# Optimization experiments

Measured on AMD Instinct MI355X. Metric: run time of the kernel, lower is better.

The kernel has to match this reference:

```python
import jax, jax.numpy as jnp
from jax import lax
import numpy as np

B = 8192   # samples
L = 32     # predicted chars per sample (num_chars[i])
M = 32     # target labels per sample (num_labels[i])
C = 96     # character classes


def _edit_trace(pred, tgt):
    """Levenshtein DP + backtrace for one sample.
    pred: [L] int, tgt: [M] int.
    Returns (ti, tj, valid) of length L+M: 1-based (i,j) positions of the
    diagonal (match/substitute) moves on the optimal edit path, as emitted by
    distance_and_trace; valid masks non-diagonal / out-of-path steps."""
    Ls, Ms = pred.shape[0], tgt.shape[0]
    cost = (pred[:, None] != tgt[None, :]).astype(jnp.int32)  # [L,M]
    row0 = jnp.arange(Ms + 1, dtype=jnp.int32)

    def row_step(prev, crow):
        first = prev[0] + 1
        def col_step(left, z):
            up, diag, c = z
            v = jnp.minimum(jnp.minimum(up + 1, left + 1), diag + c)
            return v, v
        _, rest = lax.scan(col_step, first, (prev[1:], prev[:-1], crow))
        new = jnp.concatenate([first[None], rest])
        return new, new

    _, rows = lax.scan(row_step, row0, cost)
    D = jnp.concatenate([row0[None, :], rows], axis=0)  # [L+1, M+1]

    def bt_step(carry, _):
        i, j = carry
        c = cost[jnp.maximum(i - 1, 0), jnp.maximum(j - 1, 0)]
        dij = D[i, j]
        diag = (i > 0) & (j > 0) & (D[i - 1, j - 1] + c == dij)
        up = (~diag) & (i > 0) & (D[i - 1, j] + 1 == dij)
        left = (~diag) & (~up) & (j > 0)
        ni = i - (diag | up).astype(jnp.int32)
        nj = j - (diag | left).astype(jnp.int32)
        return (ni, nj), (i, j, diag)

    (_, _), (ti, tj, valid) = lax.scan(
        bt_step, (jnp.int32(Ls), jnp.int32(Ms)), None, length=Ls + Ms)
    return ti, tj, valid


def _forward(x, y, num_chars, num_labels):
    b = num_chars.shape[0]
    c = x.shape[1]
    l = x.shape[0] // b
    m = y.shape[0] // b
    logits = x.reshape(b, l, c)          # [B,L,C]
    labels = y.reshape(b, m)             # [B,M]
    pred = jnp.argmax(logits, axis=-1)   # torch.max(x,1) indices
    ti, tj, valid = jax.vmap(_edit_trace)(pred, labels)  # [B, L+M] each
    logp = jax.nn.log_softmax(logits, axis=-1)
    xi = jnp.where(valid, ti - 1, 0)     # trace[:,0]-1 (+ per-sample offset via reshape)
    yi = jnp.where(valid, tj - 1, 0)     # trace[:,1]-1
    lab = jnp.take_along_axis(labels, yi, axis=1)                 # [B,L+M]
    lp = jnp.take_along_axis(logp, xi[..., None], axis=1)         # [B,L+M,C]
    ce = -jnp.take_along_axis(lp, lab[..., None], axis=2)[..., 0]  # [B,L+M]
    cnt = valid.sum(axis=1)
    per_sample = jnp.where(valid, ce, 0.0).sum(axis=1) / jnp.maximum(cnt, 1)
    nonempty = cnt > 0                   # attenuation: skip empty traces
    total = jnp.where(nonempty, per_sample, 0.0).sum()
    return total / nonempty.sum()


def setup_inputs() -> dict:
    key = jax.random.key(0)
    k1, k2 = jax.random.split(key)
    x = jax.random.normal(k1, (B * L, C), dtype=jnp.float32)
    y = jax.random.randint(k2, (B * M,), 0, C, dtype=jnp.int32)
    num_chars = jnp.full((B,), L, dtype=jnp.int32)
    num_labels = jnp.full((B,), M, dtype=jnp.int32)
    return {"x": x, "y": y, "num_chars": num_chars, "num_labels": num_labels}


def reference(x, y, num_chars, num_labels):
    return _forward(x, y, num_chars, num_labels)
```

## Files before the change

### kernel.cpp

```cpp
#include <hip/hip_runtime.h>
#include <stdint.h>

#define BNUM  8192
#define LROWS 32
#define MLAB  32
#define CCLS  96
#define WPB   4
#define SPW   2
#define SPB   (WPB*SPW)
#define NBLK  (BNUM/SPB)

__device__ __forceinline__ int dpp_wshr1_i32(int v) {
    return __builtin_amdgcn_update_dpp(0, v, 0x138, 0xF, 0xF, true);
}
__device__ __forceinline__ float dpp_wshr1_f32(float v) {
    return __int_as_float(
        __builtin_amdgcn_update_dpp(0, __float_as_int(v), 0x138, 0xF, 0xF, true));
}

__global__ __launch_bounds__(256, 4) void editloss_main(
    const float* __restrict__ x, const int* __restrict__ y,
    float* __restrict__ partial_sum, float* __restrict__ partial_cnt)
{
    __shared__ float  ceTab[SPB][LROWS * MLAB];
    __shared__ float2 lpS[SPB][LROWS];
    __shared__ float  psum[SPB];
    __shared__ float  pcnt[SPB];

    const int w    = threadIdx.x >> 6;
    const int lane = threadIdx.x & 63;
    const int g    = lane >> 5;
    const int u    = lane & 31;
    const int s    = w * SPW + g;
    const int sb   = blockIdx.x * SPB + s;

    const float* xs    = x + (size_t)sb * (LROWS * CCLS);
    const int    lab_u = y[sb * MLAB + u];

    {
        const float4* rowv = (const float4*)(xs + (size_t)u * CCLS);
        float bmax[4]; int bidx[4]; float bsum[4];
#pragma unroll
        for (int c = 0; c < 4; ++c) { bmax[c] = -1e30f; bidx[c] = 0; bsum[c] = 0.f; }

        float4 va[24];
#pragma unroll
        for (int t = 0; t < 24; ++t) va[t] = rowv[t];

#pragma unroll
        for (int t = 0; t < 24; ++t) {
            const int c = t / 6;
            const float4 v = va[t];
            const int base = t * 4;
            if (v.x > bmax[c]) { bmax[c] = v.x; bidx[c] = base + 0; }
            if (v.y > bmax[c]) { bmax[c] = v.y; bidx[c] = base + 1; }
            if (v.z > bmax[c]) { bmax[c] = v.z; bidx[c] = base + 2; }
            if (v.w > bmax[c]) { bmax[c] = v.w; bidx[c] = base + 3; }
            bsum[c] += __expf(v.x) + __expf(v.y) + __expf(v.z) + __expf(v.w);
        }
        float m = bmax[0]; int idx = bidx[0];
#pragma unroll
        for (int c = 1; c < 4; ++c)
            if (bmax[c] > m) { m = bmax[c]; idx = bidx[c]; }
        const float lse = __logf((bsum[0] + bsum[1]) + (bsum[2] + bsum[3]));
        lpS[s][u] = make_float2(lse, (float)idx);
    }
    asm volatile("s_waitcnt lgkmcnt(0)" ::: "memory");

    {
        const float* gcol = xs + lab_u;
#pragma unroll
        for (int r = 0; r < LROWS; ++r) {
            const float2 lp = lpS[s][r];
            const float  xg = gcol[r * CCLS];
            const float  ce = lp.x - xg;
            ceTab[s][r * MLAB + u] = ((int)lp.y == lab_u) ? ce : -ce;
        }
    }
    asm volatile("s_waitcnt lgkmcnt(0)" ::: "memory");

    const int j = u + 1;
    int   prevW = 0;   float prevCE = 0.f;
    int   diagW = 0;   float diagCE = 0.f;
#pragma unroll 4
    for (int d = 1; d <= LROWS + MLAB; ++d) {
        const int   lWs  = dpp_wshr1_i32(prevW);
        const float lCEs = dpp_wshr1_f32(prevCE);
        const int i = d - j;
        const int   lW  = (u == 0) ? max(i, 0)     : lWs;
        const float lCE = (u == 0) ? 0.f           : lCEs;
        const int   dW  = (u == 0) ? max(i - 1, 0) : diagW;
        const float dCE = (u == 0) ? 0.f           : diagCE;
        int curW; float curCE;
        if (i <= 0) {
            curW = j; curCE = 0.f;
        } else if (i > LROWS) {
            curW = prevW; curCE = prevCE;
        } else {
            const int uD = prevW & 255, uC = prevW >> 8;
            const int lD = lW & 255,    lC = lW >> 8;
            const int dD = dW & 255,    dC = dW >> 8;
            const float ct  = ceTab[s][(i - 1) * MLAB + u];
            const int   c   = (ct < 0.f) ? 1 : 0;
            const int nD = min(min(uD, lD) + 1, dD + c);
            const bool dg = (dD + c == nD);
            const bool up = !dg && (uD + 1 == nD);
            int nC; float nCE;
            if (dg)      { nC = dC + 1; nCE = dCE + fabsf(ct); }
            else if (up) { nC = uC;     nCE = prevCE;          }
            else         { nC = lC;     nCE = lCE;             }
            curW = nD | (nC << 8);
            curCE = nCE;
        }
        diagW = lWs; diagCE = lCEs;
        prevW = curW; prevCE = curCE;
    }

    if (u == 31) {
        const int cnt = prevW >> 8;
        psum[s] = (cnt > 0) ? prevCE / (float)cnt : 0.f;
        pcnt[s] = (cnt > 0) ? 1.f : 0.f;
    }
    __syncthreads();
    if (threadIdx.x == 0) {
        float ss = 0.f, cc = 0.f;
#pragma unroll
        for (int k = 0; k < SPB; ++k) { ss += psum[k]; cc += pcnt[k]; }
        partial_sum[blockIdx.x] = ss;
        partial_cnt[blockIdx.x] = cc;
    }
}

__global__ __launch_bounds__(256) void editloss_finalize(
    const float* __restrict__ partial_sum, const float* __restrict__ partial_cnt,
    float* __restrict__ out, int nblocks)
{
    float s = 0.f, c = 0.f;
    for (int k = threadIdx.x; k < nblocks; k += 256) {
        s += partial_sum[k];
        c += partial_cnt[k];
    }
#pragma unroll
    for (int d = 32; d >= 1; d >>= 1) {
        s += __shfl_xor(s, d);
        c += __shfl_xor(c, d);
    }
    __shared__ float ss[4], cc[4];
    const int w = threadIdx.x >> 6, lane = threadIdx.x & 63;
    if (lane == 0) { ss[w] = s; cc[w] = c; }
    __syncthreads();
    if (threadIdx.x == 0) {
        const float S  = ss[0] + ss[1] + ss[2] + ss[3];
        const float C2 = cc[0] + cc[1] + cc[2] + cc[3];
        out[0] = (C2 > 0.f) ? (S / C2) : 0.f;
    }
}

extern "C" void kernel_launch(void* const* d_in, const int* in_sizes, int n_in,
                              void* d_out, int out_size, void* d_ws, size_t ws_size,
                              hipStream_t stream) {
    const float* x = (const float*)d_in[0];
    const int*   y = (const int*)d_in[1];
    float* out = (float*)d_out;

    float* partial_sum = (float*)d_ws;
    float* partial_cnt = partial_sum + NBLK;

    editloss_main<<<NBLK, 256, 0, stream>>>(x, y, partial_sum, partial_cnt);
    editloss_finalize<<<1, 256, 0, stream>>>(partial_sum, partial_cnt, out, NBLK);
}
```

Measured before the change: 166.0 us.

## Stage logits through padded LDS with coalesced loads and fuse CE into DP

Switches to one-wavefront blocks of two samples. All logits are loaded with fully coalesced float4 reads into a padded shared-memory tile, replacing per-lane strided row loads and the strided label-column gather. The precomputed CE table is dropped, and CE plus the mismatch flag are computed inside the anti-diagonal DP from staged row data. The block reduction becomes a shuffle instead of a barrier. The cost is more LDS traffic inside the DP loop, scalar LDS writes during staging, and far more blocks.

```diff
diff --git a/kernel.cpp b/kernel.cpp
--- a/kernel.cpp
+++ b/kernel.cpp
@@ -5,10 +5,13 @@
 #define LROWS 32
 #define MLAB  32
 #define CCLS  96
-#define WPB   4
-#define SPW   2
-#define SPB   (WPB*SPW)
+#define SPB   2
 #define NBLK  (BNUM/SPB)
+#define PSTR  97
+#define SSTR  (LROWS*PSTR)
+#define XS_F  (SPB*SSTR)
+#define LP_F  XS_F
+#define TOT_F (XS_F + SPB*LROWS*2)
 
 __device__ __forceinline__ int dpp_wshr1_i32(int v) {
     return __builtin_amdgcn_update_dpp(0, v, 0x138, 0xF, 0xF, true);
@@ -18,75 +21,78 @@
         __builtin_amdgcn_update_dpp(0, __float_as_int(v), 0x138, 0xF, 0xF, true));
 }
 
-__global__ __launch_bounds__(256, 4) void editloss_main(
+__global__ __launch_bounds__(64, 2) void editloss_main(
     const float* __restrict__ x, const int* __restrict__ y,
     float* __restrict__ partial_sum, float* __restrict__ partial_cnt)
 {
-    __shared__ float  ceTab[SPB][LROWS * MLAB];
-    __shared__ float2 lpS[SPB][LROWS];
-    __shared__ float  psum[SPB];
-    __shared__ float  pcnt[SPB];
+    __shared__ float S[TOT_F];
 
-    const int w    = threadIdx.x >> 6;
-    const int lane = threadIdx.x & 63;
+    const int lane = threadIdx.x;
     const int g    = lane >> 5;
     const int u    = lane & 31;
-    const int s    = w * SPW + g;
-    const int sb   = blockIdx.x * SPB + s;
+    const int sb0  = blockIdx.x * SPB;
 
-    const float* xs    = x + (size_t)sb * (LROWS * CCLS);
-    const int    lab_u = y[sb * MLAB + u];
+    const float* gx    = x + (size_t)sb0 * (LROWS * CCLS);
+    const int    lab_u = y[(sb0 + g) * MLAB + u];
+
+#pragma unroll
+    for (int i = 0; i < 24; ++i) {
+        const int    f = i * 256 + lane * 4;
+        const float4 v = *(const float4*)(gx + f);
+        const int samp = (f >= 3072) ? 1 : 0;
+        const int fs   = f - samp * 3072;
+        const int n    = fs >> 5;
+        const int row  = (n * 171) >> 9;
+        const int col  = fs - row * 96;
+        float* p = &S[samp * SSTR + row * PSTR + col];
+        p[0] = v.x; p[1] = v.y; p[2] = v.z; p[3] = v.w;
+    }
+    asm volatile("s_waitcnt lgkmcnt(0)" ::: "memory");
 
     {
-        const float4* rowv = (const float4*)(xs + (size_t)u * CCLS);
+        const float* rp = &S[g * SSTR + u * PSTR];
         float bmax[4]; int bidx[4]; float bsum[4];
 #pragma unroll
         for (int c = 0; c < 4; ++c) { bmax[c] = -1e30f; bidx[c] = 0; bsum[c] = 0.f; }
-
-        float4 va[24];
-#pragma unroll
-        for (int t = 0; t < 24; ++t) va[t] = rowv[t];
-
 #pragma unroll
         for (int t = 0; t < 24; ++t) {
             const int c = t / 6;
-            const float4 v = va[t];
+            const float v0 = rp[t * 4 + 0];
+            const float v1 = rp[t * 4 + 1];
+            const float v2 = rp[t * 4 + 2];
+            const float v3 = rp[t * 4 + 3];
             const int base = t * 4;
-            if (v.x > bmax[c]) { bmax[c] = v.x; bidx[c] = base + 0; }
-            if (v.y > bmax[c]) { bmax[c] = v.y; bidx[c] = base + 1; }
-            if (v.z > bmax[c]) { bmax[c] = v.z; bidx[c] = base + 2; }
-            if (v.w > bmax[c]) { bmax[c] = v.w; bidx[c] = base + 3; }
-            bsum[c] += __expf(v.x) + __expf(v.y) + __expf(v.z) + __expf(v.w);
+            if (v0 > bmax[c]) { bmax[c] = v0; bidx[c] = base + 0; }
+            if (v1 > bmax[c]) { bmax[c] = v1; bidx[c] = base + 1; }
+            if (v2 > bmax[c]) { bmax[c] = v2; bidx[c] = base + 2; }
+            if (v3 > bmax[c]) { bmax[c] = v3; bidx[c] = base + 3; }
+            bsum[c] += __expf(v0) + __expf(v1) + __expf(v2) + __expf(v3);
         }
         float m = bmax[0]; int idx = bidx[0];
 #pragma unroll
         for (int c = 1; c < 4; ++c)
             if (bmax[c] > m) { m = bmax[c]; idx = bidx[c]; }
         const float lse = __logf((bsum[0] + bsum[1]) + (bsum[2] + bsum[3]));
-        lpS[s][u] = make_float2(lse, (float)idx);
+        S[LP_F + (g * 32 + u) * 2 + 0] = lse;
+        S[LP_F + (g * 32 + u) * 2 + 1] = (float)idx;
     }
     asm volatile("s_waitcnt lgkmcnt(0)" ::: "memory");
 
-    {
-        const float* gcol = xs + lab_u;
-#pragma unroll
-        for (int r = 0; r < LROWS; ++r) {
-            const float2 lp = lpS[s][r];
-            const float  xg = gcol[r * CCLS];
-            const float  ce = lp.x - xg;
-            ceTab[s][r * MLAB + u] = ((int)lp.y == lab_u) ? ce : -ce;
-        }
-    }
-    asm volatile("s_waitcnt lgkmcnt(0)" ::: "memory");
-
-    const int j = u + 1;
+    const int   j      = u + 1;
+    const float fl     = (float)lab_u;
+    const int   xbase  = g * SSTR + lab_u;
+    const int   lpbase = LP_F + g * 64;
     int   prevW = 0;   float prevCE = 0.f;
     int   diagW = 0;   float diagCE = 0.f;
 #pragma unroll 4
     for (int d = 1; d <= LROWS + MLAB; ++d) {
         const int   lWs  = dpp_wshr1_i32(prevW);
         const float lCEs = dpp_wshr1_f32(prevCE);
-        const int i = d - j;
+        const int i  = d - j;
+        const int ic = min(max(i - 1, 0), LROWS - 1);
+        const float xg  = S[xbase  + ic * PSTR];
+        const float lse = S[lpbase + ic * 2 + 0];
+        const float prf = S[lpbase + ic * 2 + 1];
         const int   lW  = (u == 0) ? max(i, 0)     : lWs;
         const float lCE = (u == 0) ? 0.f           : lCEs;
         const int   dW  = (u == 0) ? max(i - 1, 0) : diagW;
@@ -100,15 +106,15 @@
             const int uD = prevW & 255, uC = prevW >> 8;
             const int lD = lW & 255,    lC = lW >> 8;
             const int dD = dW & 255,    dC = dW >> 8;
-            const float ct  = ceTab[s][(i - 1) * MLAB + u];
-            const int   c   = (ct < 0.f) ? 1 : 0;
+            const float ce = lse - xg;
+            const int   c  = (prf != fl) ? 1 : 0;
             const int nD = min(min(uD, lD) + 1, dD + c);
             const bool dg = (dD + c == nD);
             const bool up = !dg && (uD + 1 == nD);
             int nC; float nCE;
-            if (dg)      { nC = dC + 1; nCE = dCE + fabsf(ct); }
-            else if (up) { nC = uC;     nCE = prevCE;          }
-            else         { nC = lC;     nCE = lCE;             }
+            if (dg)      { nC = dC + 1; nCE = dCE + ce; }
+            else if (up) { nC = uC;     nCE = prevCE;   }
+            else         { nC = lC;     nCE = lCE;      }
             curW = nD | (nC << 8);
             curCE = nCE;
         }
@@ -116,18 +122,17 @@
         prevW = curW; prevCE = curCE;
     }
 
+    float ps = 0.f, pc = 0.f;
     if (u == 31) {
         const int cnt = prevW >> 8;
-        psum[s] = (cnt > 0) ? prevCE / (float)cnt : 0.f;
-        pcnt[s] = (cnt > 0) ? 1.f : 0.f;
+        ps = (cnt > 0) ? prevCE / (float)cnt : 0.f;
+        pc = (cnt > 0) ? 1.f : 0.f;
     }
-    __syncthreads();
-    if (threadIdx.x == 0) {
-        float ss = 0.f, cc = 0.f;
-#pragma unroll
-        for (int k = 0; k < SPB; ++k) { ss += psum[k]; cc += pcnt[k]; }
-        partial_sum[blockIdx.x] = ss;
-        partial_cnt[blockIdx.x] = cc;
+    ps += __shfl_down(ps, 32);
+    pc += __shfl_down(pc, 32);
+    if (lane == 31) {
+        partial_sum[blockIdx.x] = ps;
+        partial_cnt[blockIdx.x] = pc;
     }
 }
 
@@ -166,6 +171,6 @@
     float* partial_sum = (float*)d_ws;
     float* partial_cnt = partial_sum + NBLK;
 
-    editloss_main<<<NBLK, 256, 0, stream>>>(x, y, partial_sum, partial_cnt);
+    editloss_main<<<NBLK, 64, 0, stream>>>(x, y, partial_sum, partial_cnt);
     editloss_finalize<<<1, 256, 0, stream>>>(partial_sum, partial_cnt, out, NBLK);
 }
```

After: 184.1 us. +10.8%, slower.

## Stage logits via async global-to-LDS loads with swizzle, split rows across half-waves

Applied to the files above, without the earlier changes.

Each wave now streams one sample's 32x96 logits straight into LDS with global_load_lds, using a swizzled layout to avoid bank conflicts. The row argmax and log-sum-exp is split across two half-waves and combined with a shuffle. After a barrier, half the waves exit and the rest run the DP for two samples per wave, reading labels' logits from LDS instead of global memory. Partial results are now written per sample, so the finalize kernel reduces over all 8192 samples. This aims to coalesce the global loads and drop the second strided gather, at the cost of idle waves during the DP, lower occupancy (launch bounds 3), and a larger final reduction.

```diff
diff --git a/kernel.cpp b/kernel.cpp
--- a/kernel.cpp
+++ b/kernel.cpp
@@ -5,10 +5,12 @@
 #define LROWS 32
 #define MLAB  32
 #define CCLS  96
-#define WPB   4
-#define SPW   2
-#define SPB   (WPB*SPW)
+#define SPB   4
 #define NBLK  (BNUM/SPB)
+#define XFL   (LROWS*CCLS)
+#define SFL   (XFL + 2*LROWS)
+
+typedef float f32x4 __attribute__((ext_vector_type(4)));
 
 __device__ __forceinline__ int dpp_wshr1_i32(int v) {
     return __builtin_amdgcn_update_dpp(0, v, 0x138, 0xF, 0xF, true);
@@ -18,68 +20,115 @@
         __builtin_amdgcn_update_dpp(0, __float_as_int(v), 0x138, 0xF, 0xF, true));
 }
 
-__global__ __launch_bounds__(256, 4) void editloss_main(
+__device__ __forceinline__ int swz12(int k, int r) {
+    return (k < 8) ? (k ^ (r & 7)) : (8 + ((k - 8) ^ (r & 3)));
+}
+
+__device__ __forceinline__ void gload16(const float* g, float* l) {
+    __builtin_amdgcn_global_load_lds(
+        (const __attribute__((address_space(1))) unsigned int*)g,
+        (__attribute__((address_space(3))) unsigned int*)l,
+        16, 0, 0);
+}
+
+__global__ __launch_bounds__(256, 3) void editloss_main(
     const float* __restrict__ x, const int* __restrict__ y,
     float* __restrict__ partial_sum, float* __restrict__ partial_cnt)
 {
-    __shared__ float  ceTab[SPB][LROWS * MLAB];
-    __shared__ float2 lpS[SPB][LROWS];
-    __shared__ float  psum[SPB];
-    __shared__ float  pcnt[SPB];
-
-    const int w    = threadIdx.x >> 6;
-    const int lane = threadIdx.x & 63;
-    const int g    = lane >> 5;
-    const int u    = lane & 31;
-    const int s    = w * SPW + g;
-    const int sb   = blockIdx.x * SPB + s;
-
-    const float* xs    = x + (size_t)sb * (LROWS * CCLS);
-    const int    lab_u = y[sb * MLAB + u];
+    __shared__ float S[SPB * SFL];
+
+    const int tid  = threadIdx.x;
+    const int w    = tid >> 6;
+    const int lane = tid & 63;
+    const int r    = lane & 31;
+    const int h    = lane >> 5;
+
+    const int    sb = blockIdx.x * SPB + w;
+    const float* gx = x + (size_t)sb * XFL;
+    float*       Sw = &S[w * SFL];
+
+#pragma unroll
+    for (int t = 0; t < 12; ++t) {
+        const int q   = t * 64 + lane;
+        const int rr  = (q * 683) >> 14;
+        const int rem = q - rr * 24;
+        const int hh  = (rem >= 12) ? 1 : 0;
+        const int kp  = rem - 12 * hh;
+        const int kk  = swz12(kp, rr);
+        const int G   = rr * 24 + 12 * hh + kk;
+        gload16(gx + G * 4, Sw + t * 256);
+    }
+    asm volatile("s_waitcnt vmcnt(0)" ::: "memory");
 
     {
-        const float4* rowv = (const float4*)(xs + (size_t)u * CCLS);
-        float bmax[4]; int bidx[4]; float bsum[4];
-#pragma unroll
-        for (int c = 0; c < 4; ++c) { bmax[c] = -1e30f; bidx[c] = 0; bsum[c] = 0.f; }
-
-        float4 va[24];
-#pragma unroll
-        for (int t = 0; t < 24; ++t) va[t] = rowv[t];
-
-#pragma unroll
-        for (int t = 0; t < 24; ++t) {
-            const int c = t / 6;
-            const float4 v = va[t];
-            const int base = t * 4;
-            if (v.x > bmax[c]) { bmax[c] = v.x; bidx[c] = base + 0; }
-            if (v.y > bmax[c]) { bmax[c] = v.y; bidx[c] = base + 1; }
-            if (v.z > bmax[c]) { bmax[c] = v.z; bidx[c] = base + 2; }
-            if (v.w > bmax[c]) { bmax[c] = v.w; bidx[c] = base + 3; }
-            bsum[c] += __expf(v.x) + __expf(v.y) + __expf(v.z) + __expf(v.w);
-        }
-        float m = bmax[0]; int idx = bidx[0];
-#pragma unroll
-        for (int c = 1; c < 4; ++c)
-            if (bmax[c] > m) { m = bmax[c]; idx = bidx[c]; }
-        const float lse = __logf((bsum[0] + bsum[1]) + (bsum[2] + bsum[3]));
-        lpS[s][u] = make_float2(lse, (float)idx);
+        f32x4 va[12];
+#pragma unroll
+        for (int k = 0; k < 12; ++k) {
+            const int p = r * 24 + h * 12 + swz12(k, r);
+            va[k] = *(const f32x4*)(Sw + p * 4);
+        }
+        float bmA = -1e30f, bmB = -1e30f; int biA = 0, biB = 0;
+        float bsA = 0.f, bsB = 0.f;
+#pragma unroll
+        for (int k = 0; k < 12; ++k) {
+            const f32x4 v = va[k];
+            const int base = h * 48 + k * 4;
+            if (k < 6) {
+                if (v[0] > bmA) { bmA = v[0]; biA = base + 0; }
+                if (v[1] > bmA) { bmA = v[1]; biA = base + 1; }
+                if (v[2] > bmA) { bmA = v[2]; biA = base + 2; }
+                if (v[3] > bmA) { bmA = v[3]; biA = base + 3; }
+                bsA += __expf(v[0]) + __expf(v[1]) + __expf(v[2]) + __expf(v[3]);
+            } else {
+                if (v[0] > bmB) { bmB = v[0]; biB = base + 0; }
+                if (v[1] > bmB) { bmB = v[1]; biB = base + 1; }
+                if (v[2] > bmB) { bmB = v[2]; biB = base + 2; }
+                if (v[3] > bmB) { bmB = v[3]; biB = base + 3; }
+                bsB += __expf(v[0]) + __expf(v[1]) + __expf(v[2]) + __expf(v[3]);
+            }
+        }
+        float mL = bmA; int iL = biA;
+        if (bmB > mL) { mL = bmB; iL = biB; }
+        const float sL = bsA + bsB;
+        const float mP = __shfl_xor(mL, 32);
+        const int   iP = __shfl_xor(iL, 32);
+        const float sP = __shfl_xor(sL, 32);
+        const float mLo = h ? mP : mL;  const int iLo = h ? iP : iL;
+        const float mHi = h ? mL : mP;  const int iHi = h ? iL : iP;
+        const float sLo = h ? sP : sL;  const float sHi = h ? sL : sP;
+        float m = mLo; int idx = iLo;
+        if (mHi > m) { m = mHi; idx = iHi; }
+        const float lse = __logf(sLo + sHi);
+        if (h == 0) {
+            Sw[XFL + r * 2 + 0] = lse;
+            Sw[XFL + r * 2 + 1] = (float)idx;
+        }
+    }
+    __syncthreads();
+    if (w >= 2) return;
+
+    const int    sLoc = w * 2 + h;
+    const int    samp = blockIdx.x * SPB + sLoc;
+    float*       Sg   = &S[sLoc * SFL];
+    const int    lab  = y[samp * MLAB + r];
+    {
+        const int   hh = (lab >= 48) ? 1 : 0;
+        const int   kq = (lab - 48 * hh) >> 2;
+        const int   el = lab & 3;
+        const float fl = (float)lab;
+#pragma unroll
+        for (int rr = 0; rr < LROWS; ++rr) {
+            const float lse = Sg[XFL + rr * 2 + 0];
+            const float prf = Sg[XFL + rr * 2 + 1];
+            const int   p   = rr * 24 + 12 * hh + swz12(kq, rr);
+            const float xg  = Sg[p * 4 + el];
+            const float ce  = lse - xg;
+            Sg[rr * 96 + r] = (prf == fl) ? ce : -ce;
+        }
     }
     asm volatile("s_waitcnt lgkmcnt(0)" ::: "memory");
 
-    {
-        const float* gcol = xs + lab_u;
-#pragma unroll
-        for (int r = 0; r < LROWS; ++r) {
-            const float2 lp = lpS[s][r];
-            const float  xg = gcol[r * CCLS];
-            const float  ce = lp.x - xg;
-            ceTab[s][r * MLAB + u] = ((int)lp.y == lab_u) ? ce : -ce;
-        }
-    }
-    asm volatile("s_waitcnt lgkmcnt(0)" ::: "memory");
-
-    const int j = u + 1;
+    const int j = r + 1;
     int   prevW = 0;   float prevCE = 0.f;
     int   diagW = 0;   float diagCE = 0.f;
 #pragma unroll 4
@@ -87,10 +136,10 @@
         const int   lWs  = dpp_wshr1_i32(prevW);
         const float lCEs = dpp_wshr1_f32(prevCE);
         const int i = d - j;
-        const int   lW  = (u == 0) ? max(i, 0)     : lWs;
-        const float lCE = (u == 0) ? 0.f           : lCEs;
-        const int   dW  = (u == 0) ? max(i - 1, 0) : diagW;
-        const float dCE = (u == 0) ? 0.f           : diagCE;
+        const int   lW  = (r == 0) ? max(i, 0)     : lWs;
+        const float lCE = (r == 0) ? 0.f           : lCEs;
+        const int   dW  = (r == 0) ? max(i - 1, 0) : diagW;
+        const float dCE = (r == 0) ? 0.f           : diagCE;
         int curW; float curCE;
         if (i <= 0) {
             curW = j; curCE = 0.f;
@@ -100,7 +149,7 @@
             const int uD = prevW & 255, uC = prevW >> 8;
             const int lD = lW & 255,    lC = lW >> 8;
             const int dD = dW & 255,    dC = dW >> 8;
-            const float ct  = ceTab[s][(i - 1) * MLAB + u];
+            const float ct  = Sg[(i - 1) * 96 + r];
             const int   c   = (ct < 0.f) ? 1 : 0;
             const int nD = min(min(uD, lD) + 1, dD + c);
             const bool dg = (dD + c == nD);
@@ -116,27 +165,19 @@
         prevW = curW; prevCE = curCE;
     }
 
-    if (u == 31) {
+    if (r == 31) {
         const int cnt = prevW >> 8;
-        psum[s] = (cnt > 0) ? prevCE / (float)cnt : 0.f;
-        pcnt[s] = (cnt > 0) ? 1.f : 0.f;
-    }
-    __syncthreads();
-    if (threadIdx.x == 0) {
-        float ss = 0.f, cc = 0.f;
-#pragma unroll
-        for (int k = 0; k < SPB; ++k) { ss += psum[k]; cc += pcnt[k]; }
-        partial_sum[blockIdx.x] = ss;
-        partial_cnt[blockIdx.x] = cc;
+        partial_sum[samp] = (cnt > 0) ? prevCE / (float)cnt : 0.f;
+        partial_cnt[samp] = (cnt > 0) ? 1.f : 0.f;
     }
 }
 
 __global__ __launch_bounds__(256) void editloss_finalize(
     const float* __restrict__ partial_sum, const float* __restrict__ partial_cnt,
-    float* __restrict__ out, int nblocks)
+    float* __restrict__ out, int n)
 {
     float s = 0.f, c = 0.f;
-    for (int k = threadIdx.x; k < nblocks; k += 256) {
+    for (int k = threadIdx.x; k < n; k += 256) {
         s += partial_sum[k];
         c += partial_cnt[k];
     }
@@ -164,8 +205,8 @@
     float* out = (float*)d_out;
 
     float* partial_sum = (float*)d_ws;
-    float* partial_cnt = partial_sum + NBLK;
+    float* partial_cnt = partial_sum + BNUM;
 
     editloss_main<<<NBLK, 256, 0, stream>>>(x, y, partial_sum, partial_cnt);
-    editloss_finalize<<<1, 256, 0, stream>>>(partial_sum, partial_cnt, out, NBLK);
-}
+    editloss_finalize<<<1, 256, 0, stream>>>(partial_sum, partial_cnt, out, BNUM);
+}
```

New measurement: 178.3 us. 7.4% more time.
